# Kernel tuning notes

Measured on AMD Instinct MI355X. Metric: run time of the kernel, lower is better.

The kernel has to match this reference:

```python
import jax, jax.numpy as jnp
import numpy as np

T = 4096
C = 2048
N_FEAT = 2048
NEG = -1e30  # finite stand-in for -inf so fully-masked (padding) rows stay NaN-free


def setup_inputs() -> dict:
    key = jax.random.key(0)
    kx, kw, kb = jax.random.split(key, 3)
    x = jax.random.normal(kx, (T, C), dtype=jnp.float32)
    # Dense(features=3*n_feat): kernel (C, 3*n_feat), bias (3*n_feat,)
    W = jax.random.normal(kw, (C, 3 * N_FEAT), dtype=jnp.float32) * (1.0 / np.sqrt(C))
    b = jax.random.normal(kb, (3 * N_FEAT,), dtype=jnp.float32) * 0.01
    n_padd = 128
    return {"x": x, "W": W, "b": b, "n_padd": n_padd}


def reference(x, W, b, n_padd):
    T_, _ = x.shape
    qkv = x @ W + b                      # (T, 3*n_feat)
    q, k, v = jnp.split(qkv, 3, axis=1)  # each (T, n_feat)
    scale = 1.0 / jnp.sqrt(jnp.float32(q.shape[1]))
    att = (q @ k.T) * scale              # (T, T)
    rows = jnp.arange(T_)[:, None]
    cols = jnp.arange(T_)[None, :]
    # causal AND both row/col past the left padding
    mask = (cols <= rows) & (cols >= n_padd) & (rows >= n_padd)
    att = jnp.where(mask, att, NEG)
    p = jax.nn.softmax(att, axis=1)      # stable row softmax
    # kernel only stores rows >= n_padd; padding rows are zero
    p = jnp.where(rows >= n_padd, p, 0.0)
    y = p @ v                            # (T, n_feat)
    return y
```

## Files before the change

### kernel.cpp

```cpp
#include <hip/hip_runtime.h>
#include <cstdint>


#define T_DIM 4096
#define C_DIM 2048
#define NF    2048
#define N3    6144
#define NEGV  (-1e30f)

typedef __bf16 bf16x8 __attribute__((ext_vector_type(8)));
typedef __bf16 bf16x4 __attribute__((ext_vector_type(4)));
typedef float  f32x4  __attribute__((ext_vector_type(4)));

__device__ __forceinline__ void async_cp16(const void* g, void* l) {
    __builtin_amdgcn_global_load_lds(
        reinterpret_cast<const __attribute__((address_space(1))) unsigned int*>(
            reinterpret_cast<uintptr_t>(g)),
        reinterpret_cast<__attribute__((address_space(3))) unsigned int*>(
            reinterpret_cast<uintptr_t>(l)),
        16, 0, 0);
}

__device__ __forceinline__ void gemm_loop(const __bf16* A, const __bf16* B,
                                          int lda, int ldb, int m0, int n0,
                                          int kiters, __bf16* As, __bf16* Bs,
                                          f32x4 (&acc)[4][4]) {
    if (kiters <= 0) return;
    const int t    = threadIdx.x;
    const int wv   = t >> 6;
    const int lane = t & 63;
    const int srow = t >> 3;
    const int scol = (((t & 7) ^ (srow & 7)) << 3);
    const int wm   = (wv >> 1) << 6;
    const int wn   = (wv & 1) << 6;
    const int lrow = lane & 15;
    const int kq   = lane >> 4;
    const int swz  = lrow & 7;
    const int rc0  = ((kq ^ swz) << 3);
    const int rc1  = (((kq | 4) ^ swz) << 3);

    const __bf16* ga = A + (size_t)(m0 + srow) * lda + scol;
    const __bf16* gb = B + (size_t)(n0 + srow) * ldb + scol;

    auto stage = [&](int kk, int s) {
#pragma unroll
        for (int i = 0; i < 4; ++i) {
            async_cp16(ga + kk * 64 + (size_t)(32 * i) * lda,
                       &As[s * 8192 + i * 2048 + wv * 512]);
            async_cp16(gb + kk * 64 + (size_t)(32 * i) * ldb,
                       &Bs[s * 8192 + i * 2048 + wv * 512]);
        }
    };

    stage(0, 0);
    int buf = 0;
    for (int kk = 0; kk < kiters; ++kk) {
        if (kk + 1 < kiters) {
            stage(kk + 1, buf ^ 1);
            asm volatile("s_waitcnt vmcnt(8)" ::: "memory");
        } else {
            asm volatile("s_waitcnt vmcnt(0)" ::: "memory");
        }
        __builtin_amdgcn_s_barrier();
        asm volatile("" ::: "memory");
        const __bf16* Ab = &As[buf * 8192];
        const __bf16* Bb = &Bs[buf * 8192];
#pragma unroll
        for (int kb = 0; kb < 2; ++kb) {
            const int rc = kb ? rc1 : rc0;
            bf16x8 af[4], bfr[4];
#pragma unroll
            for (int mi = 0; mi < 4; ++mi)
                af[mi] = *(const bf16x8*)&Ab[(wm + mi * 16 + lrow) * 64 + rc];
#pragma unroll
            for (int ni = 0; ni < 4; ++ni)
                bfr[ni] = *(const bf16x8*)&Bb[(wn + ni * 16 + lrow) * 64 + rc];
            __builtin_amdgcn_s_setprio(1);
#pragma unroll
            for (int mi = 0; mi < 4; ++mi)
#pragma unroll
                for (int ni = 0; ni < 4; ++ni)
                    acc[mi][ni] = __builtin_amdgcn_mfma_f32_16x16x32_bf16(
                        af[mi], bfr[ni], acc[mi][ni], 0, 0, 0);
            __builtin_amdgcn_s_setprio(0);
        }
        asm volatile("" ::: "memory");
        __builtin_amdgcn_s_barrier();
        buf ^= 1;
    }
}

__global__ void prep_kernel(const float* __restrict__ x,
                            __bf16* __restrict__ xb,
                            const float* __restrict__ W,
                            __bf16* __restrict__ Wt) {
    if (blockIdx.x < 2048) {
        const int n4 = (T_DIM * C_DIM) / 4;
        const int stride = 2048 * 256;
        for (int i = blockIdx.x * 256 + threadIdx.x; i < n4; i += stride) {
            float4 v = ((const float4*)x)[i];
            bf16x4 o;
            o[0] = (__bf16)v.x; o[1] = (__bf16)v.y;
            o[2] = (__bf16)v.z; o[3] = (__bf16)v.w;
            ((bf16x4*)xb)[i] = o;
        }
        return;
    }
    __shared__ float tile[32][33];
    const int tb = blockIdx.x - 2048;
    const int bx = (tb % (N3 / 32)) * 32;
    const int by = (tb / (N3 / 32)) * 32;
    const int tx = threadIdx.x & 31, ty = threadIdx.x >> 5;
#pragma unroll
    for (int i = 0; i < 32; i += 8)
        tile[ty + i][tx] = W[(size_t)(by + ty + i) * N3 + bx + tx];
    __syncthreads();
#pragma unroll
    for (int i = 0; i < 32; i += 8)
        Wt[(size_t)(bx + ty + i) * C_DIM + by + tx] = (__bf16)tile[tx][ty + i];
}

#define EPILOG_SETUP()                                     \
    const int t = threadIdx.x, wv = t >> 6, lane = t & 63; \
    const int wm = (wv >> 1) << 6, wn = (wv & 1) << 6;     \
    const int rq = (lane >> 4) << 2, cn = lane & 15

__global__ void __launch_bounds__(512)
qkv_gemm_kernel(const __bf16* __restrict__ xb, const __bf16* __restrict__ Wt,
                const float* __restrict__ bias, __bf16* __restrict__ qb,
                __bf16* __restrict__ kb, __bf16* __restrict__ vT) {
    __shared__ __bf16 As[2][256 * 64];
    __shared__ __bf16 Bs[2][384 * 64];

    const int t    = threadIdx.x;
    const int wv   = t >> 6;
    const int lane = t & 63;
    const int srow = t >> 3;
    const int scol = (((t & 7) ^ (srow & 7)) << 3);
    const int m0   = blockIdx.x * 256;
    const int n0   = blockIdx.y * 384;
    const int wmo  = (wv >> 2) * 128;
    const int wno  = (wv & 3) * 96;
    const int lrow = lane & 15;
    const int kq   = lane >> 4;
    const int swz  = lrow & 7;
    const int rc0  = ((kq ^ swz) << 3);
    const int rc1  = (((kq | 4) ^ swz) << 3);

    const __bf16* ga = xb + (size_t)(m0 + srow) * C_DIM + scol;
    const __bf16* gb = Wt + (size_t)(n0 + srow) * C_DIM + scol;

    f32x4 acc[8][6] = {};

    auto stage = [&](int kt, int s) {
        const __bf16* a  = ga + kt * 64;
        const __bf16* b2 = gb + kt * 64;
#pragma unroll
        for (int i = 0; i < 4; ++i)
            async_cp16(a + (size_t)(64 * i) * C_DIM, &As[s][i * 4096 + wv * 512]);
#pragma unroll
        for (int i = 0; i < 6; ++i)
            async_cp16(b2 + (size_t)(64 * i) * C_DIM, &Bs[s][i * 4096 + wv * 512]);
    };

    constexpr int KT = C_DIM / 64;
    stage(0, 0);
    int buf = 0;
    for (int kt = 0; kt < KT; ++kt) {
        if (kt + 1 < KT) {
            stage(kt + 1, buf ^ 1);
            asm volatile("s_waitcnt vmcnt(10)" ::: "memory");
        } else {
            asm volatile("s_waitcnt vmcnt(0)" ::: "memory");
        }
        __builtin_amdgcn_s_barrier();
        asm volatile("" ::: "memory");
        const __bf16* Ab = As[buf];
        const __bf16* Bb = Bs[buf];
#pragma unroll
        for (int kb2 = 0; kb2 < 2; ++kb2) {
            const int rc = kb2 ? rc1 : rc0;
            bf16x8 bfr[6];
#pragma unroll
            for (int ni = 0; ni < 6; ++ni)
                bfr[ni] = *(const bf16x8*)&Bb[(wno + ni * 16 + lrow) * 64 + rc];
            __builtin_amdgcn_s_setprio(1);
#pragma unroll
            for (int mi = 0; mi < 8; ++mi) {
                bf16x8 af = *(const bf16x8*)&Ab[(wmo + mi * 16 + lrow) * 64 + rc];
#pragma unroll
                for (int ni = 0; ni < 6; ++ni)
                    acc[mi][ni] = __builtin_amdgcn_mfma_f32_16x16x32_bf16(
                        af, bfr[ni], acc[mi][ni], 0, 0, 0);
            }
            __builtin_amdgcn_s_setprio(0);
        }
        asm volatile("" ::: "memory");
        __builtin_amdgcn_s_barrier();
        buf ^= 1;
    }

    const int rq = (lane >> 4) << 2, cn = lane & 15;
#pragma unroll
    for (int mi = 0; mi < 8; ++mi)
#pragma unroll
        for (int ni = 0; ni < 6; ++ni) {
            int col = n0 + wno + ni * 16 + cn;
            float bv = bias[col];
            if (col >= 2 * NF) {
                bf16x4 o;
#pragma unroll
                for (int r = 0; r < 4; ++r) o[r] = (__bf16)(acc[mi][ni][r] + bv);
                int row = m0 + wmo + mi * 16 + rq;
                *(bf16x4*)&vT[(size_t)(col - 2 * NF) * T_DIM + row] = o;
            } else {
#pragma unroll
                for (int r = 0; r < 4; ++r) {
                    int row = m0 + wmo + mi * 16 + rq + r;
                    float val = acc[mi][ni][r] + bv;
                    if (col < NF)
                        qb[(size_t)row * NF + col] = (__bf16)val;
                    else
                        kb[(size_t)row * NF + (col - NF)] = (__bf16)val;
                }
            }
        }
}

__global__ void __launch_bounds__(256)
sc_gemm_kernel(const __bf16* __restrict__ qb, const __bf16* __restrict__ kb,
               __bf16* __restrict__ S, const int* __restrict__ npadd_p) {
    int i = blockIdx.x;
    int mt = (int)((sqrtf(8.0f * (float)i + 1.0f) - 1.0f) * 0.5f);
    while ((mt + 1) * (mt + 2) / 2 <= i) ++mt;
    while (mt * (mt + 1) / 2 > i) --mt;
    int nt = i - mt * (mt + 1) / 2;
    const int m0 = mt * 128, n0 = nt * 128;
    const int npadd = *npadd_p;
    if (m0 + 128 <= npadd || n0 + 128 <= npadd) return;

    __shared__ __bf16 As[2 * 128 * 64];
    __shared__ __bf16 Bs[2 * 128 * 64];
    f32x4 acc[4][4] = {};
    gemm_loop(qb, kb, NF, NF, m0, n0, NF / 64, As, Bs, acc);

    const float scale = 0.022097086912079608f;
    EPILOG_SETUP();
#pragma unroll
    for (int mi = 0; mi < 4; ++mi)
#pragma unroll
        for (int ni = 0; ni < 4; ++ni) {
            int j = n0 + wn + ni * 16 + cn;
#pragma unroll
            for (int r = 0; r < 4; ++r) {
                int row = m0 + wm + mi * 16 + rq + r;
                S[(size_t)row * T_DIM + j] = (__bf16)(acc[mi][ni][r] * scale);
            }
        }
}

__global__ void __launch_bounds__(256)
softmax_kernel(const __bf16* __restrict__ S, __bf16* __restrict__ P,
               const int* __restrict__ npadd_p) {
    const int wv = threadIdx.x >> 6, lane = threadIdx.x & 63;
    const int row = blockIdx.x * 4 + wv;
    const int npadd = *npadd_p;
    __bf16* prow = P + (size_t)row * T_DIM;

    if (row < npadd) {
        bf16x8 z = {};
#pragma unroll
        for (int c = 0; c < 8; ++c) ((bf16x8*)prow)[c * 64 + lane] = z;
        return;
    }

    const __bf16* srow = S + (size_t)row * T_DIM;
    float vals[64];
    float mx = NEGV;
#pragma unroll
    for (int c = 0; c < 8; ++c) {
        if (c * 512 > row) {
#pragma unroll
            for (int e = 0; e < 8; ++e) vals[c * 8 + e] = NEGV;
            continue;
        }
        int j0 = c * 512 + lane * 8;
        bf16x8 v = ((const bf16x8*)srow)[c * 64 + lane];
#pragma unroll
        for (int e = 0; e < 8; ++e) {
            float f = (j0 + e >= npadd && j0 + e <= row) ? (float)v[e] : NEGV;
            vals[c * 8 + e] = f;
            mx = fmaxf(mx, f);
        }
    }
#pragma unroll
    for (int o = 32; o > 0; o >>= 1) mx = fmaxf(mx, __shfl_xor(mx, o));

    float sm = 0.f;
#pragma unroll
    for (int k = 0; k < 64; ++k) {
        vals[k] = exp2f((vals[k] - mx) * 1.4426950408889634f);
        sm += vals[k];
    }
#pragma unroll
    for (int o = 32; o > 0; o >>= 1) sm += __shfl_xor(sm, o);
    float inv = 1.0f / sm;

#pragma unroll
    for (int c = 0; c < 8; ++c) {
        bf16x8 o;
#pragma unroll
        for (int e = 0; e < 8; ++e) o[e] = (__bf16)(vals[c * 8 + e] * inv);
        ((bf16x8*)prow)[c * 64 + lane] = o;
    }
}

__global__ void __launch_bounds__(256)
pv_gemm_kernel(const __bf16* __restrict__ P, const __bf16* __restrict__ vT,
               float* __restrict__ out, const int* __restrict__ npadd_p) {
    const int idx = blockIdx.x;
    const int kskip = *npadd_p >> 6;
    int mt, nt, start, iters;
    bool atomic_out;
    if (idx < 256) {
        mt = idx & 15; nt = idx >> 4;
        int kt = (mt + 1) * 2 - kskip; if (kt < 0) kt = 0;
        start = kskip; iters = kt; atomic_out = false;
    } else {
        int j = idx - 256;
        mt = 16 + (j & 15); nt = (j >> 4) & 15;
        int half = j >> 8;
        int kt = (mt + 1) * 2 - kskip; if (kt < 0) kt = 0;
        int h0 = (kt + 1) >> 1;
        start = kskip + (half ? h0 : 0);
        iters = half ? kt - h0 : h0;
        atomic_out = true;
    }
    const int m0 = mt * 128, n0 = nt * 128;

    __shared__ __bf16 As[2 * 128 * 64];
    __shared__ __bf16 Bs[2 * 128 * 64];
    f32x4 acc[4][4] = {};
    gemm_loop(P + (size_t)start * 64, vT + (size_t)start * 64,
              T_DIM, T_DIM, m0, n0, iters, As, Bs, acc);

    EPILOG_SETUP();
#pragma unroll
    for (int mi = 0; mi < 4; ++mi)
#pragma unroll
        for (int ni = 0; ni < 4; ++ni) {
            int col = n0 + wn + ni * 16 + cn;
#pragma unroll
            for (int r = 0; r < 4; ++r) {
                int row = m0 + wm + mi * 16 + rq + r;
                float* p = &out[(size_t)row * NF + col];
                if (atomic_out) unsafeAtomicAdd(p, acc[mi][ni][r]);
                else            *p = acc[mi][ni][r];
            }
        }
}

extern "C" void kernel_launch(void* const* d_in, const int* in_sizes, int n_in,
                              void* d_out, int out_size, void* d_ws,
                              size_t ws_size, hipStream_t stream) {
    const float* x = (const float*)d_in[0];
    const float* W = (const float*)d_in[1];
    const float* b = (const float*)d_in[2];
    const int* npadd = (const int*)d_in[3];
    float* out = (float*)d_out;

    char* ws = (char*)d_ws;
    __bf16* xb = (__bf16*)(ws);
    __bf16* Wt = (__bf16*)(ws + (16ull << 20));
    __bf16* qb = (__bf16*)(ws + (40ull << 20));
    __bf16* kb = (__bf16*)(ws + (56ull << 20));
    __bf16* vT = (__bf16*)(ws + (72ull << 20));
    __bf16* S  = (__bf16*)(ws + (88ull << 20));
    __bf16* P  = (__bf16*)(ws + (40ull << 20));

    hipMemsetAsync(out + (size_t)2048 * NF, 0, (size_t)2048 * NF * 4, stream);

    prep_kernel<<<2048 + (N3 / 32) * (C_DIM / 32), 256, 0, stream>>>(x, xb, W, Wt);
    qkv_gemm_kernel<<<dim3(T_DIM / 256, N3 / 384), 512, 0, stream>>>(xb, Wt, b,
                                                                     qb, kb, vT);
    sc_gemm_kernel<<<528, 256, 0, stream>>>(qb, kb, S, npadd);
    softmax_kernel<<<T_DIM / 4, 256, 0, stream>>>(S, P, npadd);
    pv_gemm_kernel<<<768, 256, 0, stream>>>(P, vT, out, npadd);
}
```

Measured before the change: 341.5 us.

## Split QKV GEMM k-step into four phases interleaving prefetch and MFMA

Restructures the QKV projection GEMM main loop into four sub-phases, each loading a quarter of the fragments from LDS, syncing with a barrier, then issuing MFMAs. The next tile's global-to-LDS copies are spread across the phases (A first, then two halves of B) rather than issued all at once. A single wait on outstanding copies now sits at the end of the iteration. The aim is a ping-pong style schedule that overlaps memory traffic and LDS reads with matrix math, at the cost of more barriers per iteration.

Result: faster. 330.0 us (-3.4%).

```diff
diff --git a/kernel.cpp b/kernel.cpp
--- a/kernel.cpp
+++ b/kernel.cpp
@@ -11,6 +11,9 @@
 typedef __bf16 bf16x8 __attribute__((ext_vector_type(8)));
 typedef __bf16 bf16x4 __attribute__((ext_vector_type(4)));
 typedef float  f32x4  __attribute__((ext_vector_type(4)));
+
+#define FENCE() asm volatile("" ::: "memory")
+#define BARRIER() do { FENCE(); __builtin_amdgcn_s_barrier(); FENCE(); } while (0)
 
 __device__ __forceinline__ void async_cp16(const void* g, void* l) {
     __builtin_amdgcn_global_load_lds(
@@ -62,7 +65,7 @@
             asm volatile("s_waitcnt vmcnt(0)" ::: "memory");
         }
         __builtin_amdgcn_s_barrier();
-        asm volatile("" ::: "memory");
+        FENCE();
         const __bf16* Ab = &As[buf * 8192];
         const __bf16* Bb = &Bs[buf * 8192];
 #pragma unroll
@@ -84,7 +87,7 @@
                         af[mi], bfr[ni], acc[mi][ni], 0, 0, 0);
             __builtin_amdgcn_s_setprio(0);
         }
-        asm volatile("" ::: "memory");
+        FENCE();
         __builtin_amdgcn_s_barrier();
         buf ^= 1;
     }
@@ -152,51 +155,107 @@
 
     f32x4 acc[8][6] = {};
 
-    auto stage = [&](int kt, int s) {
-        const __bf16* a  = ga + kt * 64;
-        const __bf16* b2 = gb + kt * 64;
+    auto stageA = [&](int kt, int s) {
+        const __bf16* a = ga + kt * 64;
 #pragma unroll
         for (int i = 0; i < 4; ++i)
             async_cp16(a + (size_t)(64 * i) * C_DIM, &As[s][i * 4096 + wv * 512]);
-#pragma unroll
-        for (int i = 0; i < 6; ++i)
-            async_cp16(b2 + (size_t)(64 * i) * C_DIM, &Bs[s][i * 4096 + wv * 512]);
     };
+    auto stageB = [&](int kt, int s, int h) {
+        const __bf16* b2 = gb + kt * 64;
+#pragma unroll
+        for (int i = 0; i < 3; ++i)
+            async_cp16(b2 + (size_t)(64 * (h * 3 + i)) * C_DIM,
+                       &Bs[s][(h * 3 + i) * 4096 + wv * 512]);
+    };
 
     constexpr int KT = C_DIM / 64;
-    stage(0, 0);
+
+    stageA(0, 0); stageB(0, 0, 0); stageB(0, 0, 1);
+    asm volatile("s_waitcnt vmcnt(0)" ::: "memory");
+    BARRIER();
+
     int buf = 0;
     for (int kt = 0; kt < KT; ++kt) {
-        if (kt + 1 < KT) {
-            stage(kt + 1, buf ^ 1);
-            asm volatile("s_waitcnt vmcnt(10)" ::: "memory");
-        } else {
-            asm volatile("s_waitcnt vmcnt(0)" ::: "memory");
-        }
-        __builtin_amdgcn_s_barrier();
-        asm volatile("" ::: "memory");
         const __bf16* Ab = As[buf];
         const __bf16* Bb = Bs[buf];
-#pragma unroll
-        for (int kb2 = 0; kb2 < 2; ++kb2) {
-            const int rc = kb2 ? rc1 : rc0;
-            bf16x8 bfr[6];
+        const bool pf = (kt + 1 < KT);
+        bf16x8 bfr[6];
+
+        if (pf) stageA(kt + 1, buf ^ 1);
+        {
+            bf16x8 af[4];
 #pragma unroll
             for (int ni = 0; ni < 6; ++ni)
-                bfr[ni] = *(const bf16x8*)&Bb[(wno + ni * 16 + lrow) * 64 + rc];
+                bfr[ni] = *(const bf16x8*)&Bb[(wno + ni * 16 + lrow) * 64 + rc0];
+#pragma unroll
+            for (int mi = 0; mi < 4; ++mi)
+                af[mi] = *(const bf16x8*)&Ab[(wmo + mi * 16 + lrow) * 64 + rc0];
+            BARRIER();
             __builtin_amdgcn_s_setprio(1);
 #pragma unroll
-            for (int mi = 0; mi < 8; ++mi) {
-                bf16x8 af = *(const bf16x8*)&Ab[(wmo + mi * 16 + lrow) * 64 + rc];
+            for (int mi = 0; mi < 4; ++mi)
 #pragma unroll
                 for (int ni = 0; ni < 6; ++ni)
                     acc[mi][ni] = __builtin_amdgcn_mfma_f32_16x16x32_bf16(
-                        af, bfr[ni], acc[mi][ni], 0, 0, 0);
-            }
+                        af[mi], bfr[ni], acc[mi][ni], 0, 0, 0);
             __builtin_amdgcn_s_setprio(0);
-        }
-        asm volatile("" ::: "memory");
-        __builtin_amdgcn_s_barrier();
+            BARRIER();
+        }
+        if (pf) stageB(kt + 1, buf ^ 1, 0);
+        {
+            bf16x8 af[4];
+#pragma unroll
+            for (int mi = 0; mi < 4; ++mi)
+                af[mi] = *(const bf16x8*)&Ab[(wmo + 64 + mi * 16 + lrow) * 64 + rc0];
+            BARRIER();
+            __builtin_amdgcn_s_setprio(1);
+#pragma unroll
+            for (int mi = 0; mi < 4; ++mi)
+#pragma unroll
+                for (int ni = 0; ni < 6; ++ni)
+                    acc[4 + mi][ni] = __builtin_amdgcn_mfma_f32_16x16x32_bf16(
+                        af[mi], bfr[ni], acc[4 + mi][ni], 0, 0, 0);
+            __builtin_amdgcn_s_setprio(0);
+            BARRIER();
+        }
+        if (pf) stageB(kt + 1, buf ^ 1, 1);
+        {
+            bf16x8 af[4];
+#pragma unroll
+            for (int ni = 0; ni < 6; ++ni)
+                bfr[ni] = *(const bf16x8*)&Bb[(wno + ni * 16 + lrow) * 64 + rc1];
+#pragma unroll
+            for (int mi = 0; mi < 4; ++mi)
+                af[mi] = *(const bf16x8*)&Ab[(wmo + mi * 16 + lrow) * 64 + rc1];
+            BARRIER();
+            __builtin_amdgcn_s_setprio(1);
+#pragma unroll
+            for (int mi = 0; mi < 4; ++mi)
+#pragma unroll
+                for (int ni = 0; ni < 6; ++ni)
+                    acc[mi][ni] = __builtin_amdgcn_mfma_f32_16x16x32_bf16(
+                        af[mi], bfr[ni], acc[mi][ni], 0, 0, 0);
+            __builtin_amdgcn_s_setprio(0);
+            BARRIER();
+        }
+        {
+            bf16x8 af[4];
+#pragma unroll
+            for (int mi = 0; mi < 4; ++mi)
+                af[mi] = *(const bf16x8*)&Ab[(wmo + 64 + mi * 16 + lrow) * 64 + rc1];
+            BARRIER();
+            __builtin_amdgcn_s_setprio(1);
+#pragma unroll
+            for (int mi = 0; mi < 4; ++mi)
+#pragma unroll
+                for (int ni = 0; ni < 6; ++ni)
+                    acc[4 + mi][ni] = __builtin_amdgcn_mfma_f32_16x16x32_bf16(
+                        af[mi], bfr[ni], acc[4 + mi][ni], 0, 0, 0);
+            __builtin_amdgcn_s_setprio(0);
+            if (pf) asm volatile("s_waitcnt vmcnt(0)" ::: "memory");
+            BARRIER();
+        }
         buf ^= 1;
     }
 
```

## Software-pipeline LDS fragment loads with MFMA in both GEMM main loops

Applied to the files above, without the earlier changes.

Restructures the generic GEMM loop and the QKV projection loop so that LDS fragment reads for the next k-half (and the first half of the next tile) are issued while the current MFMAs run, using double-buffered register fragments. The global-to-LDS prefetch now waits with vmcnt(0) at the end of the iteration instead of before compute, and one barrier per iteration replaces two. This is meant to hide LDS read latency behind matrix work, at the cost of higher register pressure from the extra fragment sets, and possibly exposing global load latency at the iteration tail.

Measured after the change: 518.7 us. +51.9%, slower.

```diff
diff --git a/kernel.cpp b/kernel.cpp
--- a/kernel.cpp
+++ b/kernel.cpp
@@ -11,6 +11,9 @@
 typedef __bf16 bf16x8 __attribute__((ext_vector_type(8)));
 typedef __bf16 bf16x4 __attribute__((ext_vector_type(4)));
 typedef float  f32x4  __attribute__((ext_vector_type(4)));
+
+#define FENCE() asm volatile("" ::: "memory")
+#define BARRIER() do { FENCE(); __builtin_amdgcn_s_barrier(); FENCE(); } while (0)
 
 __device__ __forceinline__ void async_cp16(const void* g, void* l) {
     __builtin_amdgcn_global_load_lds(
@@ -51,42 +54,46 @@
                        &Bs[s * 8192 + i * 2048 + wv * 512]);
         }
     };
+    auto loadF = [&](const __bf16* Ab, const __bf16* Bb, int rc,
+                     bf16x8 (&af)[4], bf16x8 (&bfr)[4]) {
+#pragma unroll
+        for (int mi = 0; mi < 4; ++mi)
+            af[mi] = *(const bf16x8*)&Ab[(wm + mi * 16 + lrow) * 64 + rc];
+#pragma unroll
+        for (int ni = 0; ni < 4; ++ni)
+            bfr[ni] = *(const bf16x8*)&Bb[(wn + ni * 16 + lrow) * 64 + rc];
+    };
+    auto mfma16 = [&](bf16x8 (&af)[4], bf16x8 (&bfr)[4]) {
+        __builtin_amdgcn_s_setprio(1);
+#pragma unroll
+        for (int mi = 0; mi < 4; ++mi)
+#pragma unroll
+            for (int ni = 0; ni < 4; ++ni)
+                acc[mi][ni] = __builtin_amdgcn_mfma_f32_16x16x32_bf16(
+                    af[mi], bfr[ni], acc[mi][ni], 0, 0, 0);
+        __builtin_amdgcn_s_setprio(0);
+    };
+
+    bf16x8 af0[4], af1[4], bf0[4], bf1[4];
 
     stage(0, 0);
-    int buf = 0;
+    asm volatile("s_waitcnt vmcnt(0)" ::: "memory");
+    BARRIER();
+    loadF(As, Bs, rc0, af0, bf0);
+
     for (int kk = 0; kk < kiters; ++kk) {
-        if (kk + 1 < kiters) {
-            stage(kk + 1, buf ^ 1);
-            asm volatile("s_waitcnt vmcnt(8)" ::: "memory");
-        } else {
-            asm volatile("s_waitcnt vmcnt(0)" ::: "memory");
-        }
-        __builtin_amdgcn_s_barrier();
-        asm volatile("" ::: "memory");
-        const __bf16* Ab = &As[buf * 8192];
-        const __bf16* Bb = &Bs[buf * 8192];
-#pragma unroll
-        for (int kb = 0; kb < 2; ++kb) {
-            const int rc = kb ? rc1 : rc0;
-            bf16x8 af[4], bfr[4];
-#pragma unroll
-            for (int mi = 0; mi < 4; ++mi)
-                af[mi] = *(const bf16x8*)&Ab[(wm + mi * 16 + lrow) * 64 + rc];
-#pragma unroll
-            for (int ni = 0; ni < 4; ++ni)
-                bfr[ni] = *(const bf16x8*)&Bb[(wn + ni * 16 + lrow) * 64 + rc];
-            __builtin_amdgcn_s_setprio(1);
-#pragma unroll
-            for (int mi = 0; mi < 4; ++mi)
-#pragma unroll
-                for (int ni = 0; ni < 4; ++ni)
-                    acc[mi][ni] = __builtin_amdgcn_mfma_f32_16x16x32_bf16(
-                        af[mi], bfr[ni], acc[mi][ni], 0, 0, 0);
-            __builtin_amdgcn_s_setprio(0);
-        }
-        asm volatile("" ::: "memory");
-        __builtin_amdgcn_s_barrier();
-        buf ^= 1;
+        const int b = kk & 1;
+        const __bf16* Ab = &As[b * 8192];
+        const __bf16* Bb = &Bs[b * 8192];
+        const bool pf = (kk + 1 < kiters);
+        if (pf) stage(kk + 1, b ^ 1);
+        loadF(Ab, Bb, rc1, af1, bf1);
+        mfma16(af0, bf0);
+        mfma16(af1, bf1);
+        asm volatile("s_waitcnt vmcnt(0)" ::: "memory");
+        BARRIER();
+        if (pf)
+            loadF(&As[(b ^ 1) * 8192], &Bs[(b ^ 1) * 8192], rc0, af0, bf0);
     }
 }
 
@@ -162,42 +169,56 @@
         for (int i = 0; i < 6; ++i)
             async_cp16(b2 + (size_t)(64 * i) * C_DIM, &Bs[s][i * 4096 + wv * 512]);
     };
-
+    auto loadA = [&](const __bf16* Ab, int mh, int rc, bf16x8 (&af)[4]) {
+#pragma unroll
+        for (int mi = 0; mi < 4; ++mi)
+            af[mi] = *(const bf16x8*)&Ab[(wmo + mh * 64 + mi * 16 + lrow) * 64 + rc];
+    };
+    auto loadB = [&](const __bf16* Bb, int rc, bf16x8 (&bfr)[6]) {
+#pragma unroll
+        for (int ni = 0; ni < 6; ++ni)
+            bfr[ni] = *(const bf16x8*)&Bb[(wno + ni * 16 + lrow) * 64 + rc];
+    };
+    auto mfma24 = [&](bf16x8 (&af)[4], bf16x8 (&bfr)[6], int mh) {
+        __builtin_amdgcn_s_setprio(1);
+#pragma unroll
+        for (int mi = 0; mi < 4; ++mi)
+#pragma unroll
+            for (int ni = 0; ni < 6; ++ni)
+                acc[mh * 4 + mi][ni] = __builtin_amdgcn_mfma_f32_16x16x32_bf16(
+                    af[mi], bfr[ni], acc[mh * 4 + mi][ni], 0, 0, 0);
+        __builtin_amdgcn_s_setprio(0);
+    };
+
+    bf16x8 afA[4], afB[4], bfrA[6], bfrB[6];
     constexpr int KT = C_DIM / 64;
+
     stage(0, 0);
-    int buf = 0;
+    asm volatile("s_waitcnt vmcnt(0)" ::: "memory");
+    BARRIER();
+    loadA(As[0], 0, rc0, afA);
+    loadB(Bs[0], rc0, bfrA);
+
     for (int kt = 0; kt < KT; ++kt) {
-        if (kt + 1 < KT) {
-            stage(kt + 1, buf ^ 1);
-            asm volatile("s_waitcnt vmcnt(10)" ::: "memory");
-        } else {
-            asm volatile("s_waitcnt vmcnt(0)" ::: "memory");
-        }
-        __builtin_amdgcn_s_barrier();
-        asm volatile("" ::: "memory");
-        const __bf16* Ab = As[buf];
-        const __bf16* Bb = Bs[buf];
-#pragma unroll
-        for (int kb2 = 0; kb2 < 2; ++kb2) {
-            const int rc = kb2 ? rc1 : rc0;
-            bf16x8 bfr[6];
-#pragma unroll
-            for (int ni = 0; ni < 6; ++ni)
-                bfr[ni] = *(const bf16x8*)&Bb[(wno + ni * 16 + lrow) * 64 + rc];
-            __builtin_amdgcn_s_setprio(1);
-#pragma unroll
-            for (int mi = 0; mi < 8; ++mi) {
-                bf16x8 af = *(const bf16x8*)&Ab[(wmo + mi * 16 + lrow) * 64 + rc];
-#pragma unroll
-                for (int ni = 0; ni < 6; ++ni)
-                    acc[mi][ni] = __builtin_amdgcn_mfma_f32_16x16x32_bf16(
-                        af, bfr[ni], acc[mi][ni], 0, 0, 0);
-            }
-            __builtin_amdgcn_s_setprio(0);
-        }
-        asm volatile("" ::: "memory");
-        __builtin_amdgcn_s_barrier();
-        buf ^= 1;
+        const int b = kt & 1;
+        const __bf16* Ab = As[b];
+        const __bf16* Bb = Bs[b];
+        const bool pf = (kt + 1 < KT);
+        if (pf) stage(kt + 1, b ^ 1);
+        loadA(Ab, 1, rc0, afB);
+        mfma24(afA, bfrA, 0);
+        loadB(Bb, rc1, bfrB);
+        loadA(Ab, 0, rc1, afA);
+        mfma24(afB, bfrA, 1);
+        loadA(Ab, 1, rc1, afB);
+        mfma24(afA, bfrB, 0);
+        mfma24(afB, bfrB, 1);
+        asm volatile("s_waitcnt vmcnt(0)" ::: "memory");
+        BARRIER();
+        if (pf) {
+            loadA(As[b ^ 1], 0, rc0, afA);
+            loadB(Bs[b ^ 1], rc0, bfrA);
+        }
     }
 
     const int rq = (lane >> 4) << 2, cn = lane & 15;
```
